# Performance work log

Hardware: AMD Instinct MI355X
Metric: run time of the kernel (lower is better)

Reference implementation:

```python
import jax, jax.numpy as jnp
import numpy as np

ALPHA = 0.2  # LeakyReLU negative slope
NEG_INF = -9e15  # matches torch -9000000000000000.0


def setup_inputs() -> dict:
    key = jax.random.key(0)
    k1, k2, k3, k4, k5, k6 = jax.random.split(key, 6)
    N, F_in, F_out = 4096, 512, 256
    adj = jax.random.randint(k1, (N, N), 0, 2, dtype=jnp.int32)
    h = jax.random.normal(k2, (N, F_in), dtype=jnp.float32)
    # proj: Linear(F_in, F_out)
    W = jax.random.normal(k3, (F_in, F_out), dtype=jnp.float32) * (1.0 / np.sqrt(F_in))
    b = jax.random.normal(k4, (F_out,), dtype=jnp.float32) * 0.01
    # proj_a: Linear(2*F_out, 1) split into the two halves acting on src/dst features
    a1 = jax.random.normal(k5, (F_out,), dtype=jnp.float32) * (1.0 / np.sqrt(2 * F_out))
    a2 = jax.random.normal(k6, (F_out,), dtype=jnp.float32) * (1.0 / np.sqrt(2 * F_out))
    a_b = jnp.zeros((), dtype=jnp.float32)
    return {"adj": adj, "h": h, "W": W, "b": b, "a1": a1, "a2": a2, "a_b": a_b}


def reference(adj, h, W, b, a1, a2, a_b):
    # wh = proj(h): [N, F_out]
    wh = h @ W + b
    # Fused form of the N x N x 2F concat + Linear(2F,1):
    # logits[i, j] = wh[i] . a1 + wh[j] . a2 + a_b
    f_src = wh @ a1  # [N]
    f_dst = wh @ a2  # [N]
    e = jax.nn.leaky_relu(f_src[:, None] + f_dst[None, :] + a_b, negative_slope=ALPHA)
    e = jnp.where(adj > 0, e, NEG_INF)
    att = jax.nn.softmax(e, axis=-1)  # F.softmax legacy dim=1 for 2D
    # dropout: inference mode (no-op) for deterministic reference
    out = att @ wh  # [N, F_out]
    return jax.nn.elu(out)  # concat=True
```

## Files before the change

kernel.cpp:

```cpp
#include <hip/hip_runtime.h>

#define NN   4096
#define FIN  512
#define FOUT 256
#define ALPHA 0.2f

typedef __attribute__((ext_vector_type(8))) short short8;
typedef __attribute__((ext_vector_type(4))) float f32x4;
typedef unsigned short u16;

__device__ __forceinline__ u16 f2bf(float x) {
    union { float f; unsigned u; } v; v.f = x;
    unsigned r = v.u + 0x7FFF + ((v.u >> 16) & 1);
    return (u16)(r >> 16);
}

__global__ __launch_bounds__(256) void k_wt(const float* __restrict__ W,
                                            u16* __restrict__ Wt) {
    __shared__ float s[64 * 65];
    const int t  = threadIdx.x;
    const int f0 = blockIdx.x * 64;
    const int k0 = blockIdx.y * 64;
    #pragma unroll
    for (int p = 0; p < 4; ++p) {
        int q = t + 256 * p, rr = q >> 4, cc = q & 15;
        float4 w4 = *(const float4*)&W[(size_t)(k0 + rr) * FOUT + f0 + cc * 4];
        s[(cc * 4 + 0) * 65 + rr] = w4.x;
        s[(cc * 4 + 1) * 65 + rr] = w4.y;
        s[(cc * 4 + 2) * 65 + rr] = w4.z;
        s[(cc * 4 + 3) * 65 + rr] = w4.w;
    }
    __syncthreads();
    #pragma unroll
    for (int p = 0; p < 4; ++p) {
        int q = t + 256 * p, f = q >> 4, kg = q & 15;
        ushort4 o;
        o.x = f2bf(s[f * 65 + kg * 4 + 0]);
        o.y = f2bf(s[f * 65 + kg * 4 + 1]);
        o.z = f2bf(s[f * 65 + kg * 4 + 2]);
        o.w = f2bf(s[f * 65 + kg * 4 + 3]);
        *(ushort4*)&Wt[(size_t)(f0 + f) * FIN + k0 + kg * 4] = o;
    }
}

#define HS 520
__global__ __launch_bounds__(256) void k_proj(const float* __restrict__ h,
                                              const u16* __restrict__ Wt,
                                              const float* __restrict__ bias,
                                              float* __restrict__ wh,
                                              u16* __restrict__ whT) {
    __shared__ u16 s_h[32 * HS];
    const int t  = threadIdx.x;
    const int f0 = blockIdx.x * 64;
    const int i0 = blockIdx.y * 32;
    #pragma unroll
    for (int p = 0; p < 16; ++p) {
        int q = t + 256 * p, row = q >> 7, c4 = q & 127;
        float4 v = *(const float4*)&h[(size_t)(i0 + row) * FIN + c4 * 4];
        ushort4 o; o.x = f2bf(v.x); o.y = f2bf(v.y); o.z = f2bf(v.z); o.w = f2bf(v.w);
        *(ushort4*)&s_h[row * HS + c4 * 4] = o;
    }
    __syncthreads();
    const int w = t >> 6, l = t & 63, n = l & 15, quad = l >> 4;
    const int hh = w & 1, fh = w >> 1;
    f32x4 acc[2] = {{0.f,0.f,0.f,0.f},{0.f,0.f,0.f,0.f}};
    #pragma unroll
    for (int k0 = 0; k0 < FIN; k0 += 32) {
        short8 a = *(const short8*)&s_h[(hh * 16 + n) * HS + k0 + quad * 8];
        short8 b0 = *(const short8*)&Wt[(size_t)(f0 + fh * 32 + n) * FIN + k0 + quad * 8];
        short8 b1 = *(const short8*)&Wt[(size_t)(f0 + fh * 32 + 16 + n) * FIN + k0 + quad * 8];
        acc[0] = __builtin_amdgcn_mfma_f32_16x16x32_bf16(a, b0, acc[0], 0, 0, 0);
        acc[1] = __builtin_amdgcn_mfma_f32_16x16x32_bf16(a, b1, acc[1], 0, 0, 0);
    }
    u16* wt_tile = whT + (size_t)(i0 >> 5) * (FOUT * 32);
    #pragma unroll
    for (int u = 0; u < 2; ++u) {
        const int f = f0 + fh * 32 + u * 16 + n;
        const float bv = bias[f];
        #pragma unroll
        for (int r = 0; r < 4; ++r) {
            const int i = i0 + hh * 16 + quad * 4 + r;
            float val = acc[u][r] + bv;
            wh[(size_t)i * FOUT + f] = val;
            wt_tile[f * 32 + (i - i0)] = f2bf(val);
        }
    }
}

__global__ __launch_bounds__(256) void k_vec(const float* __restrict__ wh,
                                             const float* __restrict__ a1,
                                             const float* __restrict__ a2,
                                             const float* __restrict__ ab,
                                             float* __restrict__ fs,
                                             float* __restrict__ fd) {
    const int i = blockIdx.x * 4 + (threadIdx.x >> 6);
    const int t = threadIdx.x & 63;
    float4 w  = ((const float4*)(wh + (size_t)i * FOUT))[t];
    float4 v1 = ((const float4*)a1)[t];
    float4 v2 = ((const float4*)a2)[t];
    float d1 = w.x*v1.x + w.y*v1.y + w.z*v1.z + w.w*v1.w;
    float d2 = w.x*v2.x + w.y*v2.y + w.z*v2.z + w.w*v2.w;
    #pragma unroll
    for (int off = 32; off > 0; off >>= 1) {
        d1 += __shfl_down(d1, off);
        d2 += __shfl_down(d2, off);
    }
    if (t == 0) { fs[i] = d1 + ab[0]; fd[i] = d2; }
}

#define BI 32
#define TJ 64
#define PS 72
__global__ __launch_bounds__(256) void k_attn(const int* __restrict__ adj,
                                              const u16* __restrict__ whT,
                                              const float* __restrict__ fs,
                                              const float* __restrict__ fd,
                                              float* __restrict__ part,
                                              float* __restrict__ psum) {
    __shared__ u16 s_p[BI * PS];
    const int t  = threadIdx.x;
    const int i0 = blockIdx.x * BI;
    const int c  = blockIdx.y;
    const int jchunk = NN / gridDim.y;
    const int jbeg = c * jchunk, jend = jbeg + jchunk;
    const int jq = t & 15, rh = t >> 4;
    const float fs0 = fs[i0 + rh], fs1 = fs[i0 + rh + 16];
    const int w = t >> 6, l = t & 63, n = l & 15, quad = l >> 4;

    f32x4 acc[2][4] = {{{0.f,0.f,0.f,0.f},{0.f,0.f,0.f,0.f},{0.f,0.f,0.f,0.f},{0.f,0.f,0.f,0.f}},
                       {{0.f,0.f,0.f,0.f},{0.f,0.f,0.f,0.f},{0.f,0.f,0.f,0.f},{0.f,0.f,0.f,0.f}}};
    float rs0 = 0.f, rs1 = 0.f;

    int4   av0 = *(const int4*)&adj[(size_t)(i0 + rh) * NN + jbeg + jq * 4];
    int4   av1 = *(const int4*)&adj[(size_t)(i0 + rh + 16) * NN + jbeg + jq * 4];
    float4 fdv = *(const float4*)&fd[jbeg + jq * 4];

    for (int j0 = jbeg; j0 < jend; j0 += TJ) {
        ushort4 o0, o1;
        {
            float x, p;
            x = fs0 + fdv.x; x = x > 0.f ? x : ALPHA * x; p = av0.x > 0 ? __expf(x) : 0.f; o0.x = f2bf(p); rs0 += p;
            x = fs0 + fdv.y; x = x > 0.f ? x : ALPHA * x; p = av0.y > 0 ? __expf(x) : 0.f; o0.y = f2bf(p); rs0 += p;
            x = fs0 + fdv.z; x = x > 0.f ? x : ALPHA * x; p = av0.z > 0 ? __expf(x) : 0.f; o0.z = f2bf(p); rs0 += p;
            x = fs0 + fdv.w; x = x > 0.f ? x : ALPHA * x; p = av0.w > 0 ? __expf(x) : 0.f; o0.w = f2bf(p); rs0 += p;
            x = fs1 + fdv.x; x = x > 0.f ? x : ALPHA * x; p = av1.x > 0 ? __expf(x) : 0.f; o1.x = f2bf(p); rs1 += p;
            x = fs1 + fdv.y; x = x > 0.f ? x : ALPHA * x; p = av1.y > 0 ? __expf(x) : 0.f; o1.y = f2bf(p); rs1 += p;
            x = fs1 + fdv.z; x = x > 0.f ? x : ALPHA * x; p = av1.z > 0 ? __expf(x) : 0.f; o1.z = f2bf(p); rs1 += p;
            x = fs1 + fdv.w; x = x > 0.f ? x : ALPHA * x; p = av1.w > 0 ? __expf(x) : 0.f; o1.w = f2bf(p); rs1 += p;
        }
        __syncthreads();
        *(ushort4*)&s_p[rh * PS + jq * 4]        = o0;
        *(ushort4*)&s_p[(rh + 16) * PS + jq * 4] = o1;
        if (j0 + TJ < jend) {
            av0 = *(const int4*)&adj[(size_t)(i0 + rh) * NN + j0 + TJ + jq * 4];
            av1 = *(const int4*)&adj[(size_t)(i0 + rh + 16) * NN + j0 + TJ + jq * 4];
            fdv = *(const float4*)&fd[j0 + TJ + jq * 4];
        }
        short8 b[2][4];
        #pragma unroll
        for (int s = 0; s < 2; ++s) {
            const u16* tb = whT + (size_t)((j0 >> 5) + s) * (FOUT * 32) + quad * 8;
            #pragma unroll
            for (int u = 0; u < 4; ++u)
                b[s][u] = *(const short8*)&tb[(w * 64 + u * 16 + n) * 32];
        }
        __syncthreads();
        #pragma unroll
        for (int s = 0; s < 2; ++s) {
            short8 a0 = *(const short8*)&s_p[n * PS + s * 32 + quad * 8];
            short8 a1f = *(const short8*)&s_p[(16 + n) * PS + s * 32 + quad * 8];
            #pragma unroll
            for (int u = 0; u < 4; ++u) {
                acc[0][u] = __builtin_amdgcn_mfma_f32_16x16x32_bf16(a0,  b[s][u], acc[0][u], 0, 0, 0);
                acc[1][u] = __builtin_amdgcn_mfma_f32_16x16x32_bf16(a1f, b[s][u], acc[1][u], 0, 0, 0);
            }
        }
    }
    #pragma unroll
    for (int m = 8; m > 0; m >>= 1) {
        rs0 += __shfl_xor(rs0, m);
        rs1 += __shfl_xor(rs1, m);
    }
    if (jq == 0) {
        psum[(size_t)c * NN + i0 + rh]      = rs0;
        psum[(size_t)c * NN + i0 + rh + 16] = rs1;
    }
    float* pc = part + ((size_t)c * NN + i0) * FOUT;
    #pragma unroll
    for (int hf = 0; hf < 2; ++hf)
        #pragma unroll
        for (int u = 0; u < 4; ++u)
            #pragma unroll
            for (int r = 0; r < 4; ++r)
                pc[(size_t)(hf * 16 + quad * 4 + r) * FOUT + w * 64 + u * 16 + n] = acc[hf][u][r];
}

__global__ __launch_bounds__(256) void k_fin(const float* __restrict__ part,
                                             const float* __restrict__ psum,
                                             float* __restrict__ out, int C) {
    const int g = blockIdx.x * 256 + threadIdx.x;
    const int i = g >> 6;
    const size_t s4 = (size_t)NN * FOUT / 4;
    float4 a = ((const float4*)part)[g];
    float s = psum[i];
    for (int c = 1; c < C; ++c) {
        float4 bb = ((const float4*)part)[g + (size_t)c * s4];
        a.x += bb.x; a.y += bb.y; a.z += bb.z; a.w += bb.w;
        s += psum[(size_t)c * NN + i];
    }
    const float inv = 1.0f / s;
    a.x *= inv; a.y *= inv; a.z *= inv; a.w *= inv;
    a.x = a.x > 0.f ? a.x : __expf(a.x) - 1.f;
    a.y = a.y > 0.f ? a.y : __expf(a.y) - 1.f;
    a.z = a.z > 0.f ? a.z : __expf(a.z) - 1.f;
    a.w = a.w > 0.f ? a.w : __expf(a.w) - 1.f;
    ((float4*)out)[g] = a;
}

extern "C" void kernel_launch(void* const* d_in, const int* in_sizes, int n_in,
                              void* d_out, int out_size, void* d_ws, size_t ws_size,
                              hipStream_t stream) {
    const int*   adj = (const int*)  d_in[0];
    const float* h   = (const float*)d_in[1];
    const float* W   = (const float*)d_in[2];
    const float* b   = (const float*)d_in[3];
    const float* a1  = (const float*)d_in[4];
    const float* a2  = (const float*)d_in[5];
    const float* ab  = (const float*)d_in[6];
    float* out = (float*)d_out;

    auto need = [](int c) -> size_t {
        size_t fl = (size_t)NN * FOUT + 2 * NN + (size_t)c * NN + (size_t)c * NN * FOUT;
        size_t us = (size_t)FOUT * FIN + (size_t)NN * FOUT;
        return fl * 4 + us * 2;
    };
    int C = 4;
    while (C > 1 && need(C) > ws_size) C >>= 1;

    float* wh   = (float*)d_ws;
    float* fs   = wh + (size_t)NN * FOUT;
    float* fd   = fs + NN;
    float* psum = fd + NN;
    float* part = psum + (size_t)C * NN;
    u16*   Wt   = (u16*)(part + (size_t)C * NN * FOUT);
    u16*   whT  = Wt + (size_t)FOUT * FIN;

    k_wt  <<<dim3(FOUT / 64, FIN / 64), 256, 0, stream>>>(W, Wt);
    k_proj<<<dim3(FOUT / 64, NN / 32), 256, 0, stream>>>(h, Wt, b, wh, whT);
    k_vec <<<NN / 4, 256, 0, stream>>>(wh, a1, a2, ab, fs, fd);
    k_attn<<<dim3(NN / BI, C), 256, 0, stream>>>(adj, whT, fs, fd, part, psum);
    k_fin <<<(NN * FOUT / 4) / 256, 256, 0, stream>>>(part, psum, out, C);
}
```

Before: 151.3 us.

## Fuse score projection into k_proj and final reduction into k_attn

Computes the per-row source/destination attention scores inside the projection kernel as per-feature-block partial sums, which removes the fp32 wh buffer and the separate k_vec launch. The attention kernel sums those partials into shared memory (fd staged in LDS). The last-arriving j-chunk block, chosen by an atomic counter, does the cross-chunk reduction, normalisation and ELU, replacing k_fin. This saves two launches and the fp32 wh round trip, at the cost of a 16 KB LDS array per block, threadfence/atomic synchronisation and a serialized tail on the winning block.

```diff
diff --git a/kernel.cpp b/kernel.cpp
--- a/kernel.cpp
+++ b/kernel.cpp
@@ -47,12 +47,18 @@
 __global__ __launch_bounds__(256) void k_proj(const float* __restrict__ h,
                                               const u16* __restrict__ Wt,
                                               const float* __restrict__ bias,
-                                              float* __restrict__ wh,
-                                              u16* __restrict__ whT) {
-    __shared__ u16 s_h[32 * HS];
+                                              const float* __restrict__ a1,
+                                              const float* __restrict__ a2,
+                                              u16* __restrict__ whT,
+                                              float* __restrict__ psrc,
+                                              float* __restrict__ pdst,
+                                              int* __restrict__ counters) {
+    __shared__ u16   s_h[32 * HS];
+    __shared__ float s_red[4 * 32];
     const int t  = threadIdx.x;
     const int f0 = blockIdx.x * 64;
     const int i0 = blockIdx.y * 32;
+    if (blockIdx.x == 0 && t == 0) counters[blockIdx.y] = 0;
     #pragma unroll
     for (int p = 0; p < 16; ++p) {
         int q = t + 256 * p, row = q >> 7, c4 = q & 127;
@@ -66,46 +72,47 @@
     f32x4 acc[2] = {{0.f,0.f,0.f,0.f},{0.f,0.f,0.f,0.f}};
     #pragma unroll
     for (int k0 = 0; k0 < FIN; k0 += 32) {
-        short8 a = *(const short8*)&s_h[(hh * 16 + n) * HS + k0 + quad * 8];
+        short8 a  = *(const short8*)&s_h[(hh * 16 + n) * HS + k0 + quad * 8];
         short8 b0 = *(const short8*)&Wt[(size_t)(f0 + fh * 32 + n) * FIN + k0 + quad * 8];
         short8 b1 = *(const short8*)&Wt[(size_t)(f0 + fh * 32 + 16 + n) * FIN + k0 + quad * 8];
         acc[0] = __builtin_amdgcn_mfma_f32_16x16x32_bf16(a, b0, acc[0], 0, 0, 0);
         acc[1] = __builtin_amdgcn_mfma_f32_16x16x32_bf16(a, b1, acc[1], 0, 0, 0);
     }
     u16* wt_tile = whT + (size_t)(i0 >> 5) * (FOUT * 32);
+    float a1v[2], a2v[2];
+    a1v[0] = a1[f0 + fh * 32 + n];      a1v[1] = a1[f0 + fh * 32 + 16 + n];
+    a2v[0] = a2[f0 + fh * 32 + n];      a2v[1] = a2[f0 + fh * 32 + 16 + n];
+    float ps[4] = {0.f,0.f,0.f,0.f}, pd[4] = {0.f,0.f,0.f,0.f};
     #pragma unroll
     for (int u = 0; u < 2; ++u) {
         const int f = f0 + fh * 32 + u * 16 + n;
         const float bv = bias[f];
         #pragma unroll
         for (int r = 0; r < 4; ++r) {
-            const int i = i0 + hh * 16 + quad * 4 + r;
             float val = acc[u][r] + bv;
-            wh[(size_t)i * FOUT + f] = val;
-            wt_tile[f * 32 + (i - i0)] = f2bf(val);
-        }
-    }
-}
-
-__global__ __launch_bounds__(256) void k_vec(const float* __restrict__ wh,
-                                             const float* __restrict__ a1,
-                                             const float* __restrict__ a2,
-                                             const float* __restrict__ ab,
-                                             float* __restrict__ fs,
-                                             float* __restrict__ fd) {
-    const int i = blockIdx.x * 4 + (threadIdx.x >> 6);
-    const int t = threadIdx.x & 63;
-    float4 w  = ((const float4*)(wh + (size_t)i * FOUT))[t];
-    float4 v1 = ((const float4*)a1)[t];
-    float4 v2 = ((const float4*)a2)[t];
-    float d1 = w.x*v1.x + w.y*v1.y + w.z*v1.z + w.w*v1.w;
-    float d2 = w.x*v2.x + w.y*v2.y + w.z*v2.z + w.w*v2.w;
-    #pragma unroll
-    for (int off = 32; off > 0; off >>= 1) {
-        d1 += __shfl_down(d1, off);
-        d2 += __shfl_down(d2, off);
-    }
-    if (t == 0) { fs[i] = d1 + ab[0]; fd[i] = d2; }
+            wt_tile[f * 32 + hh * 16 + quad * 4 + r] = f2bf(val);
+            ps[r] += val * a1v[u];
+            pd[r] += val * a2v[u];
+        }
+    }
+    #pragma unroll
+    for (int m = 1; m < 16; m <<= 1) {
+        #pragma unroll
+        for (int r = 0; r < 4; ++r) { ps[r] += __shfl_xor(ps[r], m); pd[r] += __shfl_xor(pd[r], m); }
+    }
+    if (n == 0) {
+        #pragma unroll
+        for (int r = 0; r < 4; ++r) {
+            int il = hh * 16 + quad * 4 + r;
+            s_red[fh * 32 + il]       = ps[r];
+            s_red[64 + fh * 32 + il]  = pd[r];
+        }
+    }
+    __syncthreads();
+    if (t < 32) {
+        psrc[(size_t)blockIdx.x * NN + i0 + t] = s_red[t]      + s_red[32 + t];
+        pdst[(size_t)blockIdx.x * NN + i0 + t] = s_red[64 + t] + s_red[96 + t];
+    }
 }
 
 #define BI 32
@@ -113,29 +120,50 @@
 #define PS 72
 __global__ __launch_bounds__(256) void k_attn(const int* __restrict__ adj,
                                               const u16* __restrict__ whT,
-                                              const float* __restrict__ fs,
-                                              const float* __restrict__ fd,
+                                              const float* __restrict__ psrc,
+                                              const float* __restrict__ pdst,
+                                              const float* __restrict__ ab,
                                               float* __restrict__ part,
-                                              float* __restrict__ psum) {
-    __shared__ u16 s_p[BI * PS];
+                                              float* __restrict__ psum,
+                                              int* __restrict__ counters,
+                                              float* __restrict__ out) {
+    __shared__ u16   s_p[BI * PS];
+    __shared__ float s_fd[NN];
+    __shared__ float s_fs[BI];
+    __shared__ int   s_win;
     const int t  = threadIdx.x;
     const int i0 = blockIdx.x * BI;
     const int c  = blockIdx.y;
     const int jchunk = NN / gridDim.y;
     const int jbeg = c * jchunk, jend = jbeg + jchunk;
     const int jq = t & 15, rh = t >> 4;
-    const float fs0 = fs[i0 + rh], fs1 = fs[i0 + rh + 16];
     const int w = t >> 6, l = t & 63, n = l & 15, quad = l >> 4;
+
+    if (t < BI) {
+        s_fs[t] = psrc[i0 + t] + psrc[NN + i0 + t] + psrc[2 * NN + i0 + t]
+                + psrc[3 * NN + i0 + t] + ab[0];
+    }
+    for (int q = t; q < (jchunk >> 2); q += 256) {
+        float4 v0 = ((const float4*)&pdst[jbeg])[q];
+        float4 v1 = ((const float4*)&pdst[NN + jbeg])[q];
+        float4 v2 = ((const float4*)&pdst[2 * NN + jbeg])[q];
+        float4 v3 = ((const float4*)&pdst[3 * NN + jbeg])[q];
+        float4 o;
+        o.x = v0.x + v1.x + v2.x + v3.x; o.y = v0.y + v1.y + v2.y + v3.y;
+        o.z = v0.z + v1.z + v2.z + v3.z; o.w = v0.w + v1.w + v2.w + v3.w;
+        ((float4*)s_fd)[q] = o;
+    }
+    __syncthreads();
+    const float fs0 = s_fs[rh], fs1 = s_fs[rh + 16];
 
     f32x4 acc[2][4] = {{{0.f,0.f,0.f,0.f},{0.f,0.f,0.f,0.f},{0.f,0.f,0.f,0.f},{0.f,0.f,0.f,0.f}},
                        {{0.f,0.f,0.f,0.f},{0.f,0.f,0.f,0.f},{0.f,0.f,0.f,0.f},{0.f,0.f,0.f,0.f}}};
     float rs0 = 0.f, rs1 = 0.f;
-
-    int4   av0 = *(const int4*)&adj[(size_t)(i0 + rh) * NN + jbeg + jq * 4];
-    int4   av1 = *(const int4*)&adj[(size_t)(i0 + rh + 16) * NN + jbeg + jq * 4];
-    float4 fdv = *(const float4*)&fd[jbeg + jq * 4];
+    int4 av0 = *(const int4*)&adj[(size_t)(i0 + rh) * NN + jbeg + jq * 4];
+    int4 av1 = *(const int4*)&adj[(size_t)(i0 + rh + 16) * NN + jbeg + jq * 4];
 
     for (int j0 = jbeg; j0 < jend; j0 += TJ) {
+        float4 fdv = *(const float4*)&s_fd[(j0 - jbeg) + jq * 4];
         ushort4 o0, o1;
         {
             float x, p;
@@ -154,7 +182,6 @@
         if (j0 + TJ < jend) {
             av0 = *(const int4*)&adj[(size_t)(i0 + rh) * NN + j0 + TJ + jq * 4];
             av1 = *(const int4*)&adj[(size_t)(i0 + rh + 16) * NN + j0 + TJ + jq * 4];
-            fdv = *(const float4*)&fd[j0 + TJ + jq * 4];
         }
         short8 b[2][4];
         #pragma unroll
@@ -167,7 +194,7 @@
         __syncthreads();
         #pragma unroll
         for (int s = 0; s < 2; ++s) {
-            short8 a0 = *(const short8*)&s_p[n * PS + s * 32 + quad * 8];
+            short8 a0  = *(const short8*)&s_p[n * PS + s * 32 + quad * 8];
             short8 a1f = *(const short8*)&s_p[(16 + n) * PS + s * 32 + quad * 8];
             #pragma unroll
             for (int u = 0; u < 4; ++u) {
@@ -193,28 +220,35 @@
             #pragma unroll
             for (int r = 0; r < 4; ++r)
                 pc[(size_t)(hf * 16 + quad * 4 + r) * FOUT + w * 64 + u * 16 + n] = acc[hf][u][r];
-}
-
-__global__ __launch_bounds__(256) void k_fin(const float* __restrict__ part,
-                                             const float* __restrict__ psum,
-                                             float* __restrict__ out, int C) {
-    const int g = blockIdx.x * 256 + threadIdx.x;
-    const int i = g >> 6;
-    const size_t s4 = (size_t)NN * FOUT / 4;
-    float4 a = ((const float4*)part)[g];
-    float s = psum[i];
-    for (int c = 1; c < C; ++c) {
-        float4 bb = ((const float4*)part)[g + (size_t)c * s4];
-        a.x += bb.x; a.y += bb.y; a.z += bb.z; a.w += bb.w;
-        s += psum[(size_t)c * NN + i];
-    }
-    const float inv = 1.0f / s;
-    a.x *= inv; a.y *= inv; a.z *= inv; a.w *= inv;
-    a.x = a.x > 0.f ? a.x : __expf(a.x) - 1.f;
-    a.y = a.y > 0.f ? a.y : __expf(a.y) - 1.f;
-    a.z = a.z > 0.f ? a.z : __expf(a.z) - 1.f;
-    a.w = a.w > 0.f ? a.w : __expf(a.w) - 1.f;
-    ((float4*)out)[g] = a;
+
+    __threadfence();
+    if (t == 0) s_win = (atomicAdd(&counters[blockIdx.x], 1) == (int)gridDim.y - 1) ? 1 : 0;
+    __syncthreads();
+    if (s_win) {
+        __threadfence();
+        const int Cn = gridDim.y;
+        const size_t s4 = (size_t)NN * (FOUT / 4);
+        const float4* p4 = (const float4*)part;
+        for (int p = 0; p < 8; ++p) {
+            const int q = t + 256 * p;
+            const int il = q >> 6;
+            const size_t g = (size_t)(i0 + il) * (FOUT / 4) + (q & 63);
+            float4 a = p4[g];
+            float s = psum[i0 + il];
+            for (int cc = 1; cc < Cn; ++cc) {
+                float4 bb = p4[g + (size_t)cc * s4];
+                a.x += bb.x; a.y += bb.y; a.z += bb.z; a.w += bb.w;
+                s += psum[(size_t)cc * NN + i0 + il];
+            }
+            const float inv = 1.0f / s;
+            a.x *= inv; a.y *= inv; a.z *= inv; a.w *= inv;
+            a.x = a.x > 0.f ? a.x : __expf(a.x) - 1.f;
+            a.y = a.y > 0.f ? a.y : __expf(a.y) - 1.f;
+            a.z = a.z > 0.f ? a.z : __expf(a.z) - 1.f;
+            a.w = a.w > 0.f ? a.w : __expf(a.w) - 1.f;
+            ((float4*)out)[g] = a;
+        }
+    }
 }
 
 extern "C" void kernel_launch(void* const* d_in, const int* in_sizes, int n_in,
@@ -230,24 +264,22 @@
     float* out = (float*)d_out;
 
     auto need = [](int c) -> size_t {
-        size_t fl = (size_t)NN * FOUT + 2 * NN + (size_t)c * NN + (size_t)c * NN * FOUT;
+        size_t fl = 8 * (size_t)NN + (size_t)c * NN + (size_t)c * NN * FOUT + 128;
         size_t us = (size_t)FOUT * FIN + (size_t)NN * FOUT;
         return fl * 4 + us * 2;
     };
     int C = 4;
     while (C > 1 && need(C) > ws_size) C >>= 1;
 
-    float* wh   = (float*)d_ws;
-    float* fs   = wh + (size_t)NN * FOUT;
-    float* fd   = fs + NN;
-    float* psum = fd + NN;
+    float* psrc = (float*)d_ws;
+    float* pdst = psrc + 4 * (size_t)NN;
+    float* psum = pdst + 4 * (size_t)NN;
     float* part = psum + (size_t)C * NN;
-    u16*   Wt   = (u16*)(part + (size_t)C * NN * FOUT);
-    u16*   whT  = Wt + (size_t)FOUT * FIN;
+    int*   counters = (int*)(part + (size_t)C * NN * FOUT);
+    u16*   Wt  = (u16*)(counters + 128);
+    u16*   whT = Wt + (size_t)FOUT * FIN;
 
     k_wt  <<<dim3(FOUT / 64, FIN / 64), 256, 0, stream>>>(W, Wt);
-    k_proj<<<dim3(FOUT / 64, NN / 32), 256, 0, stream>>>(h, Wt, b, wh, whT);
-    k_vec <<<NN / 4, 256, 0, stream>>>(wh, a1, a2, ab, fs, fd);
-    k_attn<<<dim3(NN / BI, C), 256, 0, stream>>>(adj, whT, fs, fd, part, psum);
-    k_fin <<<(NN * FOUT / 4) / 256, 256, 0, stream>>>(part, psum, out, C);
-}
+    k_proj<<<dim3(FOUT / 64, NN / 32), 256, 0, stream>>>(h, Wt, b, a1, a2, whT, psrc, pdst, counters);
+    k_attn<<<dim3(NN / BI, C), 256, 0, stream>>>(adj, whT, psrc, pdst, ab, part, psum, counters, out);
+}
```

Result: slower. 242.9 us (+60.6%).
